# Optimization experiments

Measured on AMD Instinct MI355X. Metric: run time of the kernel, lower is better.

The kernel has to match this reference:

```python
import jax, jax.numpy as jnp
import numpy as np
import math

B, S, H = 8, 2048, 256

def setup_inputs() -> dict:
    key = jax.random.key(0)
    ks = jax.random.split(key, 7)
    stdv = 1.0 / math.sqrt(H)
    return {
        "k": jax.random.normal(ks[0], (B, S, H), dtype=jnp.float32),
        "q": jax.random.normal(ks[1], (B, S, H), dtype=jnp.float32),
        "v": jax.random.normal(ks[2], (B, S, H), dtype=jnp.float32),
        "mask": jax.random.bernoulli(ks[3], 0.5, (B, S, S)),  # bool, masked-out positions
        "W_query": jax.random.uniform(ks[4], (H, H), jnp.float32, -stdv, stdv),
        "W_key": jax.random.uniform(ks[5], (H, H), jnp.float32, -stdv, stdv),
        "W_val": jax.random.uniform(ks[6], (H, H), jnp.float32, -stdv, stdv),
    }

def reference(k, q, v, mask, W_query, W_key, W_val):
    Q = jnp.einsum("bsh,hd->bsd", q, W_query)
    K = jnp.einsum("bsh,hd->bsd", k, W_key)
    V = jnp.einsum("bsh,hd->bsd", v, W_val)
    norm = 1.0 / math.sqrt(Q.shape[-1])
    compat = norm * jnp.einsum("bqd,bkd->bqk", Q, K)  # [B,Sq,Sk]
    compat = jnp.where(mask, -jnp.inf, compat)
    score = jax.nn.softmax(compat, axis=-1)
    score = jnp.nan_to_num(score, nan=0.0)  # fully-masked rows -> all zeros
    return jnp.einsum("bqk,bkd->bqd", score, V)
```

## Files before the change

### kernel.cpp

```cpp
#include <hip/hip_runtime.h>


#define B_ 8
#define S_ 2048
#define H_ 256

typedef __attribute__((ext_vector_type(8))) short s16x8;
typedef __attribute__((ext_vector_type(4))) float f32x4;
typedef __attribute__((ext_vector_type(4))) unsigned short u16x4;
typedef __attribute__((ext_vector_type(8))) unsigned short u16x8;

#if __has_builtin(__builtin_amdgcn_exp2f)
#define EXP2F(x) __builtin_amdgcn_exp2f(x)
#else
#define EXP2F(x) exp2f(x)
#endif

__device__ __forceinline__ unsigned short f2bf(float f) {
  unsigned int u = __builtin_bit_cast(unsigned int, f);
  u += 0x7fffu + ((u >> 16) & 1u);
  return (unsigned short)(u >> 16);
}
__device__ __forceinline__ float bf2f(unsigned short h) {
  unsigned int u = ((unsigned int)h) << 16;
  return __builtin_bit_cast(float, u);
}
__device__ __forceinline__ f32x4 mfma_bf16(s16x8 a, s16x8 b, f32x4 c) {
  return __builtin_amdgcn_mfma_f32_16x16x32_bf16(a, b, c, 0, 0, 0);
}
__device__ __forceinline__ float sel4(const float v[4], int r) {
  float t0 = (r & 1) ? v[1] : v[0];
  float t1 = (r & 1) ? v[3] : v[2];
  return (r & 2) ? t1 : t0;
}
__device__ __forceinline__ void async16(const unsigned short* g, unsigned short* l) {
  __builtin_amdgcn_global_load_lds(
      (const __attribute__((address_space(1))) unsigned int*)g,
      (__attribute__((address_space(3))) unsigned int*)l, 16, 0, 0);
}

__global__ __launch_bounds__(256) void wt_kernel(
    const float* __restrict__ Wq, const float* __restrict__ Wk,
    const float* __restrict__ Wv, unsigned short* __restrict__ Wt) {
  __shared__ unsigned short tile[64 * 72];
  int z = blockIdx.x >> 4, x = blockIdx.x & 15;
  const float* W = (z == 0) ? Wq : (z == 1) ? Wk : Wv;
  int n0 = (x & 3) * 64, h0 = (x >> 2) * 64;
  int t = threadIdx.x;
#pragma unroll
  for (int j = 0; j < 4; ++j) {
    int c = j * 256 + t;
    int i = c >> 4, ch = c & 15;
    float4 f = *(const float4*)&W[(h0 + i) * 256 + n0 + ch * 4];
    u16x4 p;
    p[0] = f2bf(f.x); p[1] = f2bf(f.y); p[2] = f2bf(f.z); p[3] = f2bf(f.w);
    *(u16x4*)&tile[i * 72 + ch * 4] = p;
  }
  __syncthreads();
#pragma unroll
  for (int j = 0; j < 2; ++j) {
    int c = j * 256 + t;
    int nr = c >> 3, ch = c & 7;
    u16x8 o;
#pragma unroll
    for (int k = 0; k < 8; ++k) o[k] = tile[(ch * 8 + k) * 72 + nr];
    *(u16x8*)&Wt[z * 65536 + (n0 + nr) * 256 + h0 + ch * 8] = o;
  }
}

__global__ __launch_bounds__(256) void proj_kernel(
    const float* __restrict__ Xq, const float* __restrict__ Xk,
    const float* __restrict__ Xv, const unsigned short* __restrict__ Wt,
    unsigned short* __restrict__ Qb, unsigned short* __restrict__ Kb,
    unsigned short* __restrict__ Vt) {
  __shared__ unsigned short plds[16384];

  int z = blockIdx.x >> 8;
  int bx = blockIdx.x & 255;
  const float* X = (z == 0) ? Xq : (z == 1) ? Xk : Xv;
  const unsigned short* Wz = Wt + z * 65536;

  int t = threadIdx.x;
  int w = t >> 6, lane = t & 63, quad = lane >> 4, l15 = lane & 15;
  int m0 = bx * 64;
  const float* xrow = X + (size_t)(m0 + w * 16 + l15) * H_;

  f32x4 zero4 = {0.f, 0.f, 0.f, 0.f};
  f32x4 acc[16];
#pragma unroll
  for (int i = 0; i < 16; ++i) acc[i] = zero4;

#pragma unroll
  for (int j = 0; j < 4; ++j) {
    int c = j * 256 + t;
    int n = c >> 2, p = c & 3;
    async16(Wz + n * 256 + ((p ^ ((n >> 1) & 3)) << 3),
            plds + j * 2048 + w * 512);
  }
  float4 a0 = *(const float4*)(xrow + quad * 8);
  float4 a1 = *(const float4*)(xrow + quad * 8 + 4);

  for (int c8 = 0; c8 < 8; ++c8) {
    int cur = c8 & 1;
    unsigned short* Wc = plds + cur * 8192;
    __syncthreads();

    if (c8 < 7) {
      unsigned short* Wn = plds + (cur ^ 1) * 8192;
#pragma unroll
      for (int j = 0; j < 4; ++j) {
        int c = j * 256 + t;
        int n = c >> 2, p = c & 3;
        async16(Wz + n * 256 + (c8 + 1) * 32 + ((p ^ ((n >> 1) & 3)) << 3),
                Wn + j * 2048 + w * 512);
      }
    }
    float4 na0, na1;
    if (c8 < 7) {
      na0 = *(const float4*)(xrow + (c8 + 1) * 32 + quad * 8);
      na1 = *(const float4*)(xrow + (c8 + 1) * 32 + quad * 8 + 4);
    }
    s16x8 af;
    af[0] = (short)f2bf(a0.x); af[1] = (short)f2bf(a0.y);
    af[2] = (short)f2bf(a0.z); af[3] = (short)f2bf(a0.w);
    af[4] = (short)f2bf(a1.x); af[5] = (short)f2bf(a1.y);
    af[6] = (short)f2bf(a1.z); af[7] = (short)f2bf(a1.w);

#pragma unroll
    for (int nf = 0; nf < 16; ++nf) {
      int n = nf * 16 + l15;
      s16x8 bf = *(const s16x8*)&Wc[n * 32 + ((quad ^ ((n >> 1) & 3)) << 3)];
      acc[nf] = mfma_bf16(af, bf, acc[nf]);
    }
    a0 = na0; a1 = na1;
  }
  __syncthreads();

  float scale = (z == 0) ? 0.090168439f : 1.0f;
  int b = m0 >> 11, s0 = m0 & 2047;
#pragma unroll
  for (int h = 0; h < 2; ++h) {
    if (h) __syncthreads();
    if (z < 2) {
#pragma unroll
      for (int nf2 = 0; nf2 < 8; ++nf2) {
        int n = nf2 * 16 + l15;
#pragma unroll
        for (int r = 0; r < 4; ++r)
          plds[(w * 16 + quad * 4 + r) * 136 + n] = f2bf(acc[h * 8 + nf2][r] * scale);
      }
      __syncthreads();
      unsigned short* Y = (z == 0) ? Qb : Kb;
#pragma unroll
      for (int j = 0; j < 4; ++j) {
        int c = j * 256 + t;
        int mr = c >> 4, ch = c & 15;
        u16x8 o = *(const u16x8*)&plds[mr * 136 + ch * 8];
        *(u16x8*)&Y[(size_t)(m0 + mr) * H_ + h * 128 + ch * 8] = o;
      }
    } else {
#pragma unroll
      for (int nf2 = 0; nf2 < 8; ++nf2) {
        int dl = nf2 * 16 + l15;
#pragma unroll
        for (int r = 0; r < 4; ++r)
          plds[dl * 72 + (w * 16 + quad * 4 + r)] = f2bf(acc[h * 8 + nf2][r]);
      }
      __syncthreads();
#pragma unroll
      for (int j = 0; j < 4; ++j) {
        int c = j * 256 + t;
        int dr = c >> 3, ch = c & 7;
        u16x8 o = *(const u16x8*)&plds[dr * 72 + ch * 8];
        *(u16x8*)&Vt[((size_t)b * H_ + h * 128 + dr) * S_ + s0 + ch * 8] = o;
      }
    }
  }
}

__global__ __launch_bounds__(256, 2) void attn_kernel(
    const unsigned short* __restrict__ Qb, const unsigned short* __restrict__ Kb,
    const unsigned short* __restrict__ Vt, const int* __restrict__ mask,
    unsigned short* __restrict__ Op, float* __restrict__ Ml,
    float* __restrict__ out) {
  __shared__ unsigned short lds[35072];
  unsigned short* Ps = lds + 32768;

  int t = threadIdx.x;
  int w = t >> 6, lane = t & 63, quad = lane >> 4, l15 = lane & 15;
  int b = blockIdx.x;
  int q0 = blockIdx.y * 64;
  int split = blockIdx.z, nsplit = gridDim.z;
  int kbeg = (64 * split) / nsplit, kend = (64 * (split + 1)) / nsplit;

  s16x8 qa[8];
  {
    const unsigned short* qp =
        Qb + ((size_t)b * S_ + q0 + w * 16 + l15) * H_ + quad * 8;
#pragma unroll
    for (int c = 0; c < 8; ++c) qa[c] = *(const s16x8*)(qp + 32 * c);
  }

  const unsigned short* Kbb = Kb + (size_t)b * S_ * H_;
  const unsigned short* Vbb = Vt + (size_t)b * H_ * S_;

  int krow = lane >> 5, kch = lane & 31;
  int vrow = lane >> 2, vch = lane & 3;

  f32x4 zero4 = {0.f, 0.f, 0.f, 0.f};
  f32x4 acc[16];
#pragma unroll
  for (int i = 0; i < 16; ++i) acc[i] = zero4;
  float l_r[4] = {0.f, 0.f, 0.f, 0.f};

  const int* mrow[4];
#pragma unroll
  for (int r = 0; r < 4; ++r)
    mrow[r] = mask + ((size_t)b * S_ + q0 + w * 16 + quad * 4 + r) * S_;

  {
    int k0 = kbeg * 32;
    unsigned short* Kd = lds;
    unsigned short* Vd = lds + 8192;
#pragma unroll
    for (int j = 0; j < 4; ++j) {
      int key = (w * 4 + j) * 2 + krow;
      async16(Kbb + ((size_t)(k0 + key) << 8) + ((kch ^ (key & 7)) << 3),
              Kd + (w * 4 + j) * 512);
      int d = w * 64 + j * 16 + vrow;
      async16(Vbb + ((size_t)d << 11) + k0 + ((vch ^ ((d >> 1) & 3)) << 3),
              Vd + (w * 64 + j * 16) * 32);
    }
  }
  int mw[2][4];
#pragma unroll
  for (int nf = 0; nf < 2; ++nf)
#pragma unroll
    for (int r = 0; r < 4; ++r)
      mw[nf][r] = mrow[r][kbeg * 32 + nf * 16 + l15];

  for (int kt = kbeg; kt < kend; ++kt) {
    int cur = (kt - kbeg) & 1;
    unsigned short* Ksc = lds + cur * 16384;
    unsigned short* Vsc = Ksc + 8192;
    __syncthreads();

    if (kt + 1 < kend) {
      int k0 = (kt + 1) * 32;
      unsigned short* Kd = lds + (cur ^ 1) * 16384;
      unsigned short* Vd = Kd + 8192;
#pragma unroll
      for (int j = 0; j < 4; ++j) {
        int key = (w * 4 + j) * 2 + krow;
        async16(Kbb + ((size_t)(k0 + key) << 8) + ((kch ^ (key & 7)) << 3),
                Kd + (w * 4 + j) * 512);
        int d = w * 64 + j * 16 + vrow;
        async16(Vbb + ((size_t)d << 11) + k0 + ((vch ^ ((d >> 1) & 3)) << 3),
                Vd + (w * 64 + j * 16) * 32);
      }
    }
    int mwn[2][4];
    {
      int ktn = (kt + 1 < kend) ? kt + 1 : kt;
#pragma unroll
      for (int nf = 0; nf < 2; ++nf)
#pragma unroll
        for (int r = 0; r < 4; ++r)
          mwn[nf][r] = mrow[r][ktn * 32 + nf * 16 + l15];
    }

    f32x4 sacc[2];
    sacc[0] = zero4; sacc[1] = zero4;
    __builtin_amdgcn_s_setprio(1);
#pragma unroll
    for (int c = 0; c < 8; ++c) {
#pragma unroll
      for (int nf = 0; nf < 2; ++nf) {
        int n = nf * 16 + l15;
        s16x8 kb = *(const s16x8*)&Ksc[n * 256 + (((quad + 4 * c) ^ (n & 7)) << 3)];
        sacc[nf] = mfma_bf16(qa[c], kb, sacc[nf]);
      }
    }
    __builtin_amdgcn_s_setprio(0);

    float pvv[2][4];
#pragma unroll
    for (int r = 0; r < 4; ++r) {
#pragma unroll
      for (int nf = 0; nf < 2; ++nf) {
        float p = mw[nf][r] ? 0.f : EXP2F(sacc[nf][r]);
        pvv[nf][r] = p;
        l_r[r] += p;
      }
    }

#pragma unroll
    for (int nf = 0; nf < 2; ++nf)
#pragma unroll
      for (int r = 0; r < 4; ++r) {
        int key = nf * 16 + l15;
        int ql = quad * 4 + r;
        Ps[w * 576 + ql * 36 + key] = f2bf(pvv[nf][r]);
      }

    {
      s16x8 bp = *(const s16x8*)&Ps[w * 576 + l15 * 36 + quad * 8];
      __builtin_amdgcn_s_setprio(1);
#pragma unroll
      for (int mf = 0; mf < 16; ++mf) {
        int d = mf * 16 + l15;
        s16x8 av = *(const s16x8*)&Vsc[d * 32 + ((quad ^ ((d >> 1) & 3)) << 3)];
        acc[mf] = mfma_bf16(av, bp, acc[mf]);
      }
      __builtin_amdgcn_s_setprio(0);
    }

#pragma unroll
    for (int nf = 0; nf < 2; ++nf)
#pragma unroll
      for (int r = 0; r < 4; ++r) mw[nf][r] = mwn[nf][r];
  }

#pragma unroll
  for (int r = 0; r < 4; ++r) {
#pragma unroll
    for (int d = 1; d < 16; d <<= 1) l_r[r] += __shfl_xor(l_r[r], d, 64);
  }

  if (gridDim.z == 1) {
    float l4[4];
    int srcl = (l15 >> 2) << 4;
#pragma unroll
    for (int r = 0; r < 4; ++r) l4[r] = __shfl(l_r[r], srcl, 64);
    float lq = sel4(l4, l15 & 3);
    float linv = (lq > 0.f) ? (1.0f / lq) : 0.f;
    float* op = out + ((size_t)b * S_ + q0 + w * 16 + l15) * H_ + quad * 4;
#pragma unroll
    for (int mf = 0; mf < 16; ++mf) {
      float4 o;
      o.x = acc[mf][0] * linv; o.y = acc[mf][1] * linv;
      o.z = acc[mf][2] * linv; o.w = acc[mf][3] * linv;
      *(float4*)(op + mf * 16) = o;
    }
  } else {
    int qg = q0 + w * 16 + l15;
    unsigned short* op =
        Op + (((size_t)split * B_ + b) * S_ + qg) * H_ + quad * 4;
#pragma unroll
    for (int mf = 0; mf < 16; ++mf) {
      u16x4 pk;
      pk[0] = f2bf(acc[mf][0]); pk[1] = f2bf(acc[mf][1]);
      pk[2] = f2bf(acc[mf][2]); pk[3] = f2bf(acc[mf][3]);
      *(u16x4*)(op + mf * 16) = pk;
    }
    if (l15 == 0) {
#pragma unroll
      for (int r = 0; r < 4; ++r) {
        int qr = q0 + w * 16 + quad * 4 + r;
        Ml[((size_t)split * B_ + b) * S_ + qr] = l_r[r];
      }
    }
  }
}

__global__ __launch_bounds__(1024) void combine_kernel(
    const unsigned short* __restrict__ Op, const float* __restrict__ Ml,
    float* __restrict__ out, int nsplit) {
  int q = blockIdx.x * 4 + (threadIdx.x >> 8);
  int b = blockIdx.y, d = threadIdx.x & 255;
  float osum = 0.f, lsum = 0.f;
  for (int i = 0; i < nsplit; ++i) {
    size_t ro = ((size_t)i * B_ + b) * S_ + q;
    lsum += Ml[ro];
    osum += bf2f(Op[ro * H_ + d]);
  }
  float linv = (lsum > 0.f) ? (1.0f / lsum) : 0.f;
  out[((size_t)b * S_ + q) * H_ + d] = osum * linv;
}

extern "C" void kernel_launch(void* const* d_in, const int* in_sizes, int n_in,
                              void* d_out, int out_size, void* d_ws, size_t ws_size,
                              hipStream_t stream) {
  const float* k_in = (const float*)d_in[0];
  const float* q_in = (const float*)d_in[1];
  const float* v_in = (const float*)d_in[2];
  const int* mask = (const int*)d_in[3];
  const float* Wq = (const float*)d_in[4];
  const float* Wk = (const float*)d_in[5];
  const float* Wv = (const float*)d_in[6];
  float* out = (float*)d_out;

  unsigned short* Qb = (unsigned short*)d_ws;
  unsigned short* Kb = Qb + (size_t)4194304;
  unsigned short* Vt = Kb + (size_t)4194304;
  unsigned short* Wt = Vt + (size_t)4194304;
  unsigned short* Op = Wt + (size_t)196608;
  float* Ml = (float*)(Op + (size_t)8388608);
  const size_t need = 42467328;
  int nsplit = (ws_size >= need) ? 2 : 1;

  hipLaunchKernelGGL(wt_kernel, dim3(48), dim3(256), 0, stream,
                     Wq, Wk, Wv, Wt);
  hipLaunchKernelGGL(proj_kernel, dim3(768), dim3(256), 0, stream,
                     q_in, k_in, v_in, Wt, Qb, Kb, Vt);
  hipLaunchKernelGGL(attn_kernel, dim3(8, 32, nsplit), dim3(256), 0, stream,
                     Qb, Kb, Vt, mask, Op, Ml, out);
  if (nsplit > 1)
    hipLaunchKernelGGL(combine_kernel, dim3(512, 8), dim3(1024), 0, stream,
                       Op, Ml, out, nsplit);
}
```

Before: 291.5 us.

## Repartition attention waves into 2x2 query/key split with shared P tile

Reassigns the four waves from owning 16 query rows each to a 2x2 split: each wave computes scores for 32 queries against 16 keys, then after a block barrier computes PV for all 64 queries over a 64-wide slice of the head dimension. This lets each K fragment and V fragment loaded from LDS feed several MFMAs instead of one, cutting LDS read traffic per MFMA. In exchange it adds an extra __syncthreads per key tile and an LDS reduction of the row sums across the two key-half waves, and doubles the Q fragments held in registers.

```diff
diff --git a/kernel.cpp b/kernel.cpp
--- a/kernel.cpp
+++ b/kernel.cpp
@@ -27,11 +27,6 @@
 }
 __device__ __forceinline__ f32x4 mfma_bf16(s16x8 a, s16x8 b, f32x4 c) {
   return __builtin_amdgcn_mfma_f32_16x16x32_bf16(a, b, c, 0, 0, 0);
-}
-__device__ __forceinline__ float sel4(const float v[4], int r) {
-  float t0 = (r & 1) ? v[1] : v[0];
-  float t1 = (r & 1) ? v[3] : v[2];
-  return (r & 2) ? t1 : t0;
 }
 __device__ __forceinline__ void async16(const unsigned short* g, unsigned short* l) {
   __builtin_amdgcn_global_load_lds(
@@ -183,22 +178,25 @@
     const unsigned short* __restrict__ Vt, const int* __restrict__ mask,
     unsigned short* __restrict__ Op, float* __restrict__ Ml,
     float* __restrict__ out) {
-  __shared__ unsigned short lds[35072];
+  __shared__ unsigned short lds[35328];
   unsigned short* Ps = lds + 32768;
+  float* lsumf = (float*)(lds + 35072);
 
   int t = threadIdx.x;
   int w = t >> 6, lane = t & 63, quad = lane >> 4, l15 = lane & 15;
+  int hq = w >> 1, hk = w & 1;
   int b = blockIdx.x;
   int q0 = blockIdx.y * 64;
   int split = blockIdx.z, nsplit = gridDim.z;
   int kbeg = (64 * split) / nsplit, kend = (64 * (split + 1)) / nsplit;
 
-  s16x8 qa[8];
-  {
+  s16x8 qa[2][8];
+#pragma unroll
+  for (int qf = 0; qf < 2; ++qf) {
     const unsigned short* qp =
-        Qb + ((size_t)b * S_ + q0 + w * 16 + l15) * H_ + quad * 8;
-#pragma unroll
-    for (int c = 0; c < 8; ++c) qa[c] = *(const s16x8*)(qp + 32 * c);
+        Qb + ((size_t)b * S_ + q0 + hq * 32 + qf * 16 + l15) * H_ + quad * 8;
+#pragma unroll
+    for (int c = 0; c < 8; ++c) qa[qf][c] = *(const s16x8*)(qp + 32 * c);
   }
 
   const unsigned short* Kbb = Kb + (size_t)b * S_ * H_;
@@ -208,15 +206,20 @@
   int vrow = lane >> 2, vch = lane & 3;
 
   f32x4 zero4 = {0.f, 0.f, 0.f, 0.f};
-  f32x4 acc[16];
-#pragma unroll
-  for (int i = 0; i < 16; ++i) acc[i] = zero4;
-  float l_r[4] = {0.f, 0.f, 0.f, 0.f};
-
-  const int* mrow[4];
-#pragma unroll
-  for (int r = 0; r < 4; ++r)
-    mrow[r] = mask + ((size_t)b * S_ + q0 + w * 16 + quad * 4 + r) * S_;
+  f32x4 acc[4][4];
+#pragma unroll
+  for (int i = 0; i < 4; ++i)
+#pragma unroll
+    for (int j = 0; j < 4; ++j) acc[i][j] = zero4;
+  float l_r[2][4] = {{0.f, 0.f, 0.f, 0.f}, {0.f, 0.f, 0.f, 0.f}};
+
+  const int* mrow[2][4];
+#pragma unroll
+  for (int qf = 0; qf < 2; ++qf)
+#pragma unroll
+    for (int r = 0; r < 4; ++r)
+      mrow[qf][r] =
+          mask + ((size_t)b * S_ + q0 + hq * 32 + qf * 16 + quad * 4 + r) * S_;
 
   {
     int k0 = kbeg * 32;
@@ -234,10 +237,10 @@
   }
   int mw[2][4];
 #pragma unroll
-  for (int nf = 0; nf < 2; ++nf)
+  for (int qf = 0; qf < 2; ++qf)
 #pragma unroll
     for (int r = 0; r < 4; ++r)
-      mw[nf][r] = mrow[r][kbeg * 32 + nf * 16 + l15];
+      mw[qf][r] = mrow[qf][r][kbeg * 32 + hk * 16 + l15];
 
   for (int kt = kbeg; kt < kend; ++kt) {
     int cur = (kt - kbeg) & 1;
@@ -263,10 +266,10 @@
     {
       int ktn = (kt + 1 < kend) ? kt + 1 : kt;
 #pragma unroll
-      for (int nf = 0; nf < 2; ++nf)
+      for (int qf = 0; qf < 2; ++qf)
 #pragma unroll
         for (int r = 0; r < 4; ++r)
-          mwn[nf][r] = mrow[r][ktn * 32 + nf * 16 + l15];
+          mwn[qf][r] = mrow[qf][r][ktn * 32 + hk * 16 + l15];
     }
 
     f32x4 sacc[2];
@@ -274,91 +277,100 @@
     __builtin_amdgcn_s_setprio(1);
 #pragma unroll
     for (int c = 0; c < 8; ++c) {
-#pragma unroll
-      for (int nf = 0; nf < 2; ++nf) {
-        int n = nf * 16 + l15;
-        s16x8 kb = *(const s16x8*)&Ksc[n * 256 + (((quad + 4 * c) ^ (n & 7)) << 3)];
-        sacc[nf] = mfma_bf16(qa[c], kb, sacc[nf]);
-      }
+      int n = hk * 16 + l15;
+      s16x8 kb = *(const s16x8*)&Ksc[n * 256 + (((quad + 4 * c) ^ (n & 7)) << 3)];
+#pragma unroll
+      for (int qf = 0; qf < 2; ++qf)
+        sacc[qf] = mfma_bf16(qa[qf][c], kb, sacc[qf]);
     }
     __builtin_amdgcn_s_setprio(0);
 
-    float pvv[2][4];
+#pragma unroll
+    for (int qf = 0; qf < 2; ++qf)
+#pragma unroll
+      for (int r = 0; r < 4; ++r) {
+        float p = mw[qf][r] ? 0.f : EXP2F(sacc[qf][r]);
+        l_r[qf][r] += p;
+        int q = hq * 32 + qf * 16 + quad * 4 + r;
+        Ps[q * 36 + hk * 16 + l15] = f2bf(p);
+      }
+
+    __syncthreads();
+
+    {
+      s16x8 bp[4], av[4];
+#pragma unroll
+      for (int qf = 0; qf < 4; ++qf)
+        bp[qf] = *(const s16x8*)&Ps[(qf * 16 + l15) * 36 + quad * 8];
+#pragma unroll
+      for (int df = 0; df < 4; ++df) {
+        int d = w * 64 + df * 16 + l15;
+        av[df] = *(const s16x8*)&Vsc[d * 32 + ((quad ^ ((d >> 1) & 3)) << 3)];
+      }
+      __builtin_amdgcn_s_setprio(1);
+#pragma unroll
+      for (int df = 0; df < 4; ++df)
+#pragma unroll
+        for (int qf = 0; qf < 4; ++qf)
+          acc[df][qf] = mfma_bf16(av[df], bp[qf], acc[df][qf]);
+      __builtin_amdgcn_s_setprio(0);
+    }
+
+#pragma unroll
+    for (int qf = 0; qf < 2; ++qf)
+#pragma unroll
+      for (int r = 0; r < 4; ++r) mw[qf][r] = mwn[qf][r];
+  }
+
+#pragma unroll
+  for (int qf = 0; qf < 2; ++qf)
 #pragma unroll
     for (int r = 0; r < 4; ++r) {
 #pragma unroll
-      for (int nf = 0; nf < 2; ++nf) {
-        float p = mw[nf][r] ? 0.f : EXP2F(sacc[nf][r]);
-        pvv[nf][r] = p;
-        l_r[r] += p;
-      }
-    }
-
-#pragma unroll
-    for (int nf = 0; nf < 2; ++nf)
-#pragma unroll
-      for (int r = 0; r < 4; ++r) {
-        int key = nf * 16 + l15;
-        int ql = quad * 4 + r;
-        Ps[w * 576 + ql * 36 + key] = f2bf(pvv[nf][r]);
-      }
-
-    {
-      s16x8 bp = *(const s16x8*)&Ps[w * 576 + l15 * 36 + quad * 8];
-      __builtin_amdgcn_s_setprio(1);
-#pragma unroll
-      for (int mf = 0; mf < 16; ++mf) {
-        int d = mf * 16 + l15;
-        s16x8 av = *(const s16x8*)&Vsc[d * 32 + ((quad ^ ((d >> 1) & 3)) << 3)];
-        acc[mf] = mfma_bf16(av, bp, acc[mf]);
-      }
-      __builtin_amdgcn_s_setprio(0);
-    }
-
-#pragma unroll
-    for (int nf = 0; nf < 2; ++nf)
-#pragma unroll
-      for (int r = 0; r < 4; ++r) mw[nf][r] = mwn[nf][r];
-  }
-
-#pragma unroll
-  for (int r = 0; r < 4; ++r) {
-#pragma unroll
-    for (int d = 1; d < 16; d <<= 1) l_r[r] += __shfl_xor(l_r[r], d, 64);
-  }
+      for (int d = 1; d < 16; d <<= 1)
+        l_r[qf][r] += __shfl_xor(l_r[qf][r], d, 64);
+    }
+  __syncthreads();
+  if (l15 == 0) {
+#pragma unroll
+    for (int qf = 0; qf < 2; ++qf)
+#pragma unroll
+      for (int r = 0; r < 4; ++r)
+        lsumf[hk * 64 + hq * 32 + qf * 16 + quad * 4 + r] = l_r[qf][r];
+  }
+  __syncthreads();
 
   if (gridDim.z == 1) {
-    float l4[4];
-    int srcl = (l15 >> 2) << 4;
-#pragma unroll
-    for (int r = 0; r < 4; ++r) l4[r] = __shfl(l_r[r], srcl, 64);
-    float lq = sel4(l4, l15 & 3);
-    float linv = (lq > 0.f) ? (1.0f / lq) : 0.f;
-    float* op = out + ((size_t)b * S_ + q0 + w * 16 + l15) * H_ + quad * 4;
-#pragma unroll
-    for (int mf = 0; mf < 16; ++mf) {
-      float4 o;
-      o.x = acc[mf][0] * linv; o.y = acc[mf][1] * linv;
-      o.z = acc[mf][2] * linv; o.w = acc[mf][3] * linv;
-      *(float4*)(op + mf * 16) = o;
+#pragma unroll
+    for (int qf = 0; qf < 4; ++qf) {
+      float lq = lsumf[qf * 16 + l15] + lsumf[64 + qf * 16 + l15];
+      float linv = (lq > 0.f) ? (1.0f / lq) : 0.f;
+      float* op =
+          out + ((size_t)b * S_ + q0 + qf * 16 + l15) * H_ + w * 64 + quad * 4;
+#pragma unroll
+      for (int df = 0; df < 4; ++df) {
+        float4 o;
+        o.x = acc[df][qf][0] * linv; o.y = acc[df][qf][1] * linv;
+        o.z = acc[df][qf][2] * linv; o.w = acc[df][qf][3] * linv;
+        *(float4*)(op + df * 16) = o;
+      }
     }
   } else {
-    int qg = q0 + w * 16 + l15;
-    unsigned short* op =
-        Op + (((size_t)split * B_ + b) * S_ + qg) * H_ + quad * 4;
-#pragma unroll
-    for (int mf = 0; mf < 16; ++mf) {
-      u16x4 pk;
-      pk[0] = f2bf(acc[mf][0]); pk[1] = f2bf(acc[mf][1]);
-      pk[2] = f2bf(acc[mf][2]); pk[3] = f2bf(acc[mf][3]);
-      *(u16x4*)(op + mf * 16) = pk;
-    }
-    if (l15 == 0) {
-#pragma unroll
-      for (int r = 0; r < 4; ++r) {
-        int qr = q0 + w * 16 + quad * 4 + r;
-        Ml[((size_t)split * B_ + b) * S_ + qr] = l_r[r];
-      }
+#pragma unroll
+    for (int qf = 0; qf < 4; ++qf) {
+      unsigned short* op =
+          Op + (((size_t)split * B_ + b) * S_ + q0 + qf * 16 + l15) * H_ +
+          w * 64 + quad * 4;
+#pragma unroll
+      for (int df = 0; df < 4; ++df) {
+        u16x4 pk;
+        pk[0] = f2bf(acc[df][qf][0]); pk[1] = f2bf(acc[df][qf][1]);
+        pk[2] = f2bf(acc[df][qf][2]); pk[3] = f2bf(acc[df][qf][3]);
+        *(u16x4*)(op + df * 16) = pk;
+      }
+    }
+    if (t < 64) {
+      Ml[((size_t)split * B_ + b) * S_ + q0 + t] = lsumf[t] + lsumf[64 + t];
     }
   }
 }
```

New measurement: 296.9 us. About the same (+1.8%).
